# Kernel tuning notes

Measured on AMD Instinct MI355X. Metric: run time of the kernel, lower is better.

## Reference

```python
import jax, jax.numpy as jnp
import numpy as np
import math

NUM_HEADS = 16


def setup_inputs() -> dict:
    key = jax.random.key(0)
    ks = jax.random.split(key, 7)
    B, S, D = 2, 2048, 1024
    scale = 1.0 / math.sqrt(D)
    return {
        "query": jax.random.normal(ks[0], (B, S, D), jnp.float32),
        "key": jax.random.normal(ks[1], (B, S, D), jnp.float32),
        "value": jax.random.normal(ks[2], (B, S, D), jnp.float32),
        "Wq": jax.random.normal(ks[3], (D, D), jnp.float32) * scale,
        "Wk": jax.random.normal(ks[4], (D, D), jnp.float32) * scale,
        "Wv": jax.random.normal(ks[5], (D, D), jnp.float32) * scale,
        "Wo": jax.random.normal(ks[6], (D, D), jnp.float32) * scale,
    }


def reference(query, key, value, Wq, Wk, Wv, Wo):
    B, Sq, D = query.shape
    Sk = key.shape[1]
    H = NUM_HEADS
    dk = D // H
    # torch Linear (no bias): y = x @ W.T
    q = (query @ Wq.T).reshape(B, Sq, H, dk).transpose(0, 2, 1, 3)  # [B,H,Sq,dk]
    k = (key @ Wk.T).reshape(B, Sk, H, dk).transpose(0, 2, 1, 3)
    v = (value @ Wv.T).reshape(B, Sk, H, dk).transpose(0, 2, 1, 3)
    scores = jnp.einsum("bhqd,bhkd->bhqk", q, k) / jnp.sqrt(jnp.float32(dk))
    causal = jnp.tril(jnp.ones((Sq, Sk), dtype=bool))  # mask_future=True
    scores = jnp.where(causal[None, None], scores, jnp.float32(-1e9))
    p = jax.nn.softmax(scores, axis=-1)
    x = jnp.einsum("bhqk,bhkd->bhqd", p, v)  # [B,H,Sq,dk]
    x = x.transpose(0, 2, 1, 3).reshape(B, Sq, D)
    return x @ Wo.T
```

## Files before the change

kernel.cpp:

```cpp
#include <hip/hip_runtime.h>
#include <hip/hip_bf16.h>
#include <stdint.h>

#define D_MODEL 1024
#define NHEADS  16
#define DK      64
#define SEQ     2048
#define BATCH   2

typedef __bf16 bf16x8 __attribute__((ext_vector_type(8)));
typedef __bf16 bf16x4 __attribute__((ext_vector_type(4)));
typedef float  f32x4  __attribute__((ext_vector_type(4)));

__device__ __forceinline__ void async_copy16(const void* g, void* l) {
  __builtin_amdgcn_global_load_lds(
      (__attribute__((address_space(1))) void*)g,
      (__attribute__((address_space(3))) void*)l, 16, 0, 0);
}

__global__ void cast_all(const float* __restrict__ q, const float* __restrict__ k,
                         const float* __restrict__ v, const float* __restrict__ wq,
                         const float* __restrict__ wk, const float* __restrict__ wv,
                         const float* __restrict__ wo,
                         __bf16* __restrict__ oq, __bf16* __restrict__ ok,
                         __bf16* __restrict__ ov, __bf16* __restrict__ owq,
                         __bf16* __restrict__ owk, __bf16* __restrict__ owv,
                         __bf16* __restrict__ owo) {
  constexpr unsigned Q4 = (unsigned)(BATCH * SEQ * D_MODEL) / 4;
  constexpr unsigned W4 = (unsigned)(D_MODEL * D_MODEL) / 4;
  unsigned i = blockIdx.x * 256u + threadIdx.x;
  const float* in; __bf16* out; unsigned off;
  if (i < 3 * Q4) {
    unsigned z = i >> 20; off = i & (Q4 - 1);
    in  = z == 0 ? q : z == 1 ? k : v;
    out = z == 0 ? oq : z == 1 ? ok : ov;
  } else {
    unsigned j = i - 3 * Q4;
    unsigned z = j >> 18; off = j & (W4 - 1);
    in  = z == 0 ? wq : z == 1 ? wk : z == 2 ? wv : wo;
    out = z == 0 ? owq : z == 1 ? owk : z == 2 ? owv : owo;
  }
  float4 val = *(const float4*)(in + (size_t)off * 4);
  bf16x4 o;
  o.x = (__bf16)val.x; o.y = (__bf16)val.y; o.z = (__bf16)val.z; o.w = (__bf16)val.w;
  *(bf16x4*)(out + (size_t)off * 4) = o;
}

__global__ __launch_bounds__(256, 3)
void gemm_proj(const __bf16* __restrict__ A0, const __bf16* __restrict__ A1, const __bf16* __restrict__ A2,
               const __bf16* __restrict__ B0, const __bf16* __restrict__ B1, const __bf16* __restrict__ B2,
               __bf16* __restrict__ Qp, __bf16* __restrict__ Kp, __bf16* __restrict__ Vt) {
  constexpr int K = D_MODEL, N = D_MODEL;
  const int zi = blockIdx.z;
  const __bf16* A; const __bf16* Bm;
  if (zi == 0)      { A = A0; Bm = B0; }
  else if (zi == 1) { A = A1; Bm = B1; }
  else              { A = A2; Bm = B2; }

  __shared__ __align__(16) char smem[34816];
  __bf16* Ash = (__bf16*)smem;
  __bf16* Bsh = (__bf16*)(smem + 16384);
  __bf16* Tr  = (__bf16*)smem;

  const int tid  = threadIdx.x;
  const int lane = tid & 63;
  const int w    = tid >> 6;
  const int quad = lane >> 4;
  const int l16  = lane & 15;
  const int wr   = w >> 1, wc = w & 1;
  const size_t m0 = (size_t)blockIdx.x * 128;
  const size_t n0 = (size_t)blockIdx.y * 128;

  f32x4 acc[4][4] = {};

  for (int k0 = 0; k0 < K; k0 += 64) {
#pragma unroll
    for (int it = 0; it < 4; ++it) {
      int slot = tid + it * 256;
      int row = slot >> 3, ch = slot & 7;
      async_copy16(A + (m0 + row) * K + k0 + ((ch ^ (row & 7)) * 8), &Ash[slot * 8]);
    }
#pragma unroll
    for (int it = 0; it < 4; ++it) {
      int slot = tid + it * 256;
      int row = slot >> 3, ch = slot & 7;
      async_copy16(Bm + (n0 + row) * K + k0 + ((ch ^ (row & 7)) * 8), &Bsh[slot * 8]);
    }
    __syncthreads();
#pragma unroll
    for (int kk = 0; kk < 2; ++kk) {
      bf16x8 af[4], bfr[4];
#pragma unroll
      for (int i = 0; i < 4; ++i) {
        int row = wr * 64 + i * 16 + l16;
        af[i] = *(const bf16x8*)&Ash[row * 64 + (((kk * 4 + quad) ^ (row & 7)) * 8)];
      }
#pragma unroll
      for (int j = 0; j < 4; ++j) {
        int row = wc * 64 + j * 16 + l16;
        bfr[j] = *(const bf16x8*)&Bsh[row * 64 + (((kk * 4 + quad) ^ (row & 7)) * 8)];
      }
#pragma unroll
      for (int i = 0; i < 4; ++i)
#pragma unroll
        for (int j = 0; j < 4; ++j)
          acc[i][j] = __builtin_amdgcn_mfma_f32_16x16x32_bf16(af[i], bfr[j], acc[i][j], 0, 0, 0);
    }
    __syncthreads();
  }

  if (zi != 2) {
    __bf16* C = (zi == 0) ? Qp : Kp;
#pragma unroll
    for (int i = 0; i < 4; ++i)
#pragma unroll
      for (int j = 0; j < 4; ++j)
#pragma unroll
        for (int r = 0; r < 4; ++r) {
          size_t row = m0 + wr * 64 + i * 16 + quad * 4 + r;
          size_t col = n0 + wc * 64 + j * 16 + l16;
          C[row * N + col] = (__bf16)acc[i][j][r];
        }
  } else {
#pragma unroll
    for (int i = 0; i < 4; ++i)
#pragma unroll
      for (int j = 0; j < 4; ++j)
#pragma unroll
        for (int r = 0; r < 4; ++r)
          Tr[(wc * 64 + j * 16 + l16) * 136 + (wr * 64 + i * 16 + quad * 4 + r)] =
              (__bf16)acc[i][j][r];
    __syncthreads();
    const int b_  = (int)(m0 >> 11);
    const int sl0 = (int)(m0 & 2047);
#pragma unroll
    for (int it = 0; it < 8; ++it) {
      int slot = tid + it * 256;
      int d = slot >> 4, sc = slot & 15;
      *(int4*)&Vt[((size_t)(b_ * D_MODEL) + n0 + d) * SEQ + sl0 + sc * 8] =
          *(const int4*)&Tr[d * 136 + sc * 8];
    }
  }
}

__global__ __launch_bounds__(256, 2)
void gemm_out(const __bf16* __restrict__ A, const __bf16* __restrict__ Bm,
              float* __restrict__ C) {
  constexpr int BM = 64, BN = 128, K = D_MODEL, N = D_MODEL;
  __shared__ __bf16 Ash[BM * 64];
  __shared__ __bf16 Bsh[BN * 64];

  const int tid  = threadIdx.x;
  const int lane = tid & 63;
  const int w    = tid >> 6;
  const int quad = lane >> 4;
  const int l16  = lane & 15;
  const int wr   = w >> 1, wc = w & 1;
  const size_t m0 = (size_t)blockIdx.x * BM;
  const size_t n0 = (size_t)blockIdx.y * BN;

  f32x4 acc[2][4] = {};

  for (int k0 = 0; k0 < K; k0 += 64) {
#pragma unroll
    for (int it = 0; it < 2; ++it) {
      int slot = tid + it * 256;
      int row = slot >> 3, ch = slot & 7;
      async_copy16(A + (m0 + row) * K + k0 + ((ch ^ (row & 7)) * 8), &Ash[slot * 8]);
    }
#pragma unroll
    for (int it = 0; it < 4; ++it) {
      int slot = tid + it * 256;
      int row = slot >> 3, ch = slot & 7;
      async_copy16(Bm + (n0 + row) * K + k0 + ((ch ^ (row & 7)) * 8), &Bsh[slot * 8]);
    }
    __syncthreads();
#pragma unroll
    for (int kk = 0; kk < 2; ++kk) {
      bf16x8 af[2], bfr[4];
#pragma unroll
      for (int i = 0; i < 2; ++i) {
        int row = wr * 32 + i * 16 + l16;
        af[i] = *(const bf16x8*)&Ash[row * 64 + (((kk * 4 + quad) ^ (row & 7)) * 8)];
      }
#pragma unroll
      for (int j = 0; j < 4; ++j) {
        int row = wc * 64 + j * 16 + l16;
        bfr[j] = *(const bf16x8*)&Bsh[row * 64 + (((kk * 4 + quad) ^ (row & 7)) * 8)];
      }
#pragma unroll
      for (int i = 0; i < 2; ++i)
#pragma unroll
        for (int j = 0; j < 4; ++j)
          acc[i][j] = __builtin_amdgcn_mfma_f32_16x16x32_bf16(af[i], bfr[j], acc[i][j], 0, 0, 0);
    }
    __syncthreads();
  }

#pragma unroll
  for (int i = 0; i < 2; ++i)
#pragma unroll
    for (int j = 0; j < 4; ++j)
#pragma unroll
      for (int r = 0; r < 4; ++r) {
        size_t row = m0 + wr * 32 + i * 16 + quad * 4 + r;
        size_t col = n0 + wc * 64 + j * 16 + l16;
        C[row * N + col] = acc[i][j][r];
      }
}

__global__ __launch_bounds__(256, 4)
void attn_kernel(const __bf16* __restrict__ Qp, const __bf16* __restrict__ Kp,
                 const __bf16* __restrict__ Vt, __bf16* __restrict__ Xo) {
  __shared__ __align__(16) char smem[32768];
  __bf16* Kb = (__bf16*)smem;
  __bf16* Vb = (__bf16*)(smem + 16384);
  float*  Xch = (float*)smem;
  float*  Ls  = (float*)(smem + 8448);

  const int tid  = threadIdx.x;
  const int lane = tid & 63;
  const int w    = tid >> 6;
  const int qh   = w >> 1, kh = w & 1;
  const int quad = lane >> 4;
  const int l16  = lane & 15;
  const int bh   = blockIdx.x;
  const int qt   = 31 - blockIdx.y;
  const int b    = bh >> 4, h = bh & 15;
  const int q0   = qt * 64;
  const size_t baseRow = (size_t)b * SEQ;
  const int colBase = h * DK;

  const int srow = w * 16 + (lane >> 2);
  const int sk   = (lane & 3) * 8;
  const int skz  = (((lane & 3) ^ ((lane >> 3) & 3)) * 8);
  const int swz  = (l16 >> 1) & 3;

  const float c1 = 0.18033688011f;
  const float c2 = -23.083120654f;

  bf16x8 aq[2][2];
  {
    const __bf16* qrow = Qp + (baseRow + q0 + qh * 32 + l16) * D_MODEL + colBase;
#pragma unroll
    for (int mt = 0; mt < 2; ++mt)
#pragma unroll
      for (int kd = 0; kd < 2; ++kd)
        aq[mt][kd] = *(const bf16x8*)(qrow + (size_t)mt * 16 * D_MODEL + kd * 32 + quad * 8);
  }

  f32x4 oacc[2][4] = {};
  float plsum[2] = {};

  const int e1 = (((quad >> 1) ^ swz) * 8) + (quad & 1) * 4;
  const int e2 = ((((quad >> 1) + 2) ^ swz) * 8) + (quad & 1) * 4;

  {
    const __bf16* kbase = Kp + (baseRow + srow) * D_MODEL + colBase + skz;
    async_copy16(kbase,      &Kb[0 * 2048 + srow * 32 + sk]);
    async_copy16(kbase + 32, &Kb[1 * 2048 + srow * 32 + sk]);
    const __bf16* vbase = Vt + ((size_t)b * D_MODEL + colBase + srow) * SEQ + skz;
    async_copy16(vbase,      &Vb[0 * 2048 + srow * 32 + sk]);
    async_copy16(vbase + 32, &Vb[1 * 2048 + srow * 32 + sk]);
  }

  for (int j = 0; j <= qt; ++j) {
    const int bf = j & 1;
    __syncthreads();

    if (j < qt) {
      const int nb = bf ^ 1;
      const __bf16* kbase = Kp + (baseRow + (size_t)(j + 1) * 64 + srow) * D_MODEL + colBase + skz;
      async_copy16(kbase,      &Kb[(nb * 2 + 0) * 2048 + srow * 32 + sk]);
      async_copy16(kbase + 32, &Kb[(nb * 2 + 1) * 2048 + srow * 32 + sk]);
      const __bf16* vbase = Vt + ((size_t)b * D_MODEL + colBase + srow) * SEQ + (size_t)(j + 1) * 64 + skz;
      async_copy16(vbase,      &Vb[(nb * 2 + 0) * 2048 + srow * 32 + sk]);
      async_copy16(vbase + 32, &Vb[(nb * 2 + 1) * 2048 + srow * 32 + sk]);
    }

    f32x4 sacc[2][2] = {};
    __builtin_amdgcn_s_setprio(1);
#pragma unroll
    for (int kd = 0; kd < 2; ++kd) {
      bf16x8 bk0 = *(const bf16x8*)&Kb[(bf * 2 + kd) * 2048 + (kh * 32 + l16) * 32 + (quad ^ swz) * 8];
      bf16x8 bk1 = *(const bf16x8*)&Kb[(bf * 2 + kd) * 2048 + (kh * 32 + 16 + l16) * 32 + (quad ^ swz) * 8];
      sacc[0][0] = __builtin_amdgcn_mfma_f32_16x16x32_bf16(bk0, aq[0][kd], sacc[0][0], 0, 0, 0);
      sacc[0][1] = __builtin_amdgcn_mfma_f32_16x16x32_bf16(bk0, aq[1][kd], sacc[0][1], 0, 0, 0);
      sacc[1][0] = __builtin_amdgcn_mfma_f32_16x16x32_bf16(bk1, aq[0][kd], sacc[1][0], 0, 0, 0);
      sacc[1][1] = __builtin_amdgcn_mfma_f32_16x16x32_bf16(bk1, aq[1][kd], sacc[1][1], 0, 0, 0);
    }
    __builtin_amdgcn_s_setprio(0);

    const bool diag = (j == qt);
    bf16x8 pa[2];
#pragma unroll
    for (int mt = 0; mt < 2; ++mt)
#pragma unroll
      for (int st = 0; st < 2; ++st)
#pragma unroll
        for (int r = 0; r < 4; ++r) {
          float arg = fmaf(sacc[st][mt][r], c1, c2);
          if (diag) {
            int rowg = q0 + qh * 32 + mt * 16 + l16;
            int colg = j * 64 + kh * 32 + st * 16 + quad * 4 + r;
            if (colg > rowg) arg = -1e30f;
          }
          float p = __builtin_amdgcn_exp2f(arg);
          plsum[mt] += p;
          pa[mt][st * 4 + r] = (__bf16)p;
        }

    __builtin_amdgcn_s_setprio(1);
#pragma unroll
    for (int nt = 0; nt < 4; ++nt) {
      const int rowb = (bf * 2 + kh) * 2048 + (nt * 16 + l16) * 32;
      bf16x4 lo = *(const bf16x4*)&Vb[rowb + e1];
      bf16x4 hi = *(const bf16x4*)&Vb[rowb + e2];
      bf16x8 bv;
      bv[0] = lo[0]; bv[1] = lo[1]; bv[2] = lo[2]; bv[3] = lo[3];
      bv[4] = hi[0]; bv[5] = hi[1]; bv[6] = hi[2]; bv[7] = hi[3];
      oacc[0][nt] = __builtin_amdgcn_mfma_f32_16x16x32_bf16(pa[0], bv, oacc[0][nt], 0, 0, 0);
      oacc[1][nt] = __builtin_amdgcn_mfma_f32_16x16x32_bf16(pa[1], bv, oacc[1][nt], 0, 0, 0);
    }
    __builtin_amdgcn_s_setprio(0);
  }

  float lred[2];
#pragma unroll
  for (int mt = 0; mt < 2; ++mt) {
    float l = plsum[mt];
    l += __shfl_xor(l, 16, 64);
    l += __shfl_xor(l, 32, 64);
    lred[mt] = l;
  }

#pragma unroll
  for (int mt = 0; mt < 2; ++mt) {
    __syncthreads();
    if (kh == 1) {
#pragma unroll
      for (int nt = 0; nt < 4; ++nt)
#pragma unroll
        for (int r = 0; r < 4; ++r)
          Xch[(qh * 16 + quad * 4 + r) * 66 + nt * 16 + l16] = oacc[mt][nt][r];
    }
    if (quad == 0) Ls[kh * 32 + qh * 16 + l16] = lred[mt];
    __syncthreads();
    if (kh == 0) {
#pragma unroll
      for (int r = 0; r < 4; ++r) {
        float lt  = Ls[0 * 32 + qh * 16 + quad * 4 + r] + Ls[1 * 32 + qh * 16 + quad * 4 + r];
        float inv = 1.0f / lt;
        size_t row = baseRow + q0 + qh * 32 + mt * 16 + quad * 4 + r;
#pragma unroll
        for (int nt = 0; nt < 4; ++nt) {
          float o = oacc[mt][nt][r] + Xch[(qh * 16 + quad * 4 + r) * 66 + nt * 16 + l16];
          Xo[row * D_MODEL + colBase + nt * 16 + l16] = (__bf16)(o * inv);
        }
      }
    }
  }
}

extern "C" void kernel_launch(void* const* d_in, const int* in_sizes, int n_in,
                              void* d_out, int out_size, void* d_ws, size_t ws_size,
                              hipStream_t stream) {
  const float* q  = (const float*)d_in[0];
  const float* k  = (const float*)d_in[1];
  const float* v  = (const float*)d_in[2];
  const float* wq = (const float*)d_in[3];
  const float* wk = (const float*)d_in[4];
  const float* wv = (const float*)d_in[5];
  const float* wo = (const float*)d_in[6];
  float* out = (float*)d_out;

  const size_t MD = (size_t)BATCH * SEQ * D_MODEL;
  const size_t WD = (size_t)D_MODEL * D_MODEL;
  __bf16* ws  = (__bf16*)d_ws;
  __bf16* Qp  = ws;
  __bf16* Kp  = Qp + MD;
  __bf16* Vt  = Kp + MD;
  __bf16* Xa  = Vt + MD;
  __bf16* qbf = Xa + MD;
  __bf16* kbf = qbf + MD;
  __bf16* vbf = kbf + MD;
  __bf16* wqb = vbf + MD;
  __bf16* wkb = wqb + WD;
  __bf16* wvb = wkb + WD;
  __bf16* wob = wvb + WD;

  cast_all<<<16384, 256, 0, stream>>>(q, k, v, wq, wk, wv, wo,
                                      qbf, kbf, vbf, wqb, wkb, wvb, wob);

  gemm_proj<<<dim3(32, 8, 3), 256, 0, stream>>>(
      qbf, kbf, vbf, wqb, wkb, wvb, Qp, Kp, Vt);

  attn_kernel<<<dim3(BATCH * NHEADS, 32), 256, 0, stream>>>(Qp, Kp, Vt, Xa);

  gemm_out<<<dim3(64, 8), 256, 0, stream>>>(Xa, wob, out);
}
```

Baseline: 182.6 us.

## Fuse all four stages into one persistent cooperative kernel with grid syncs

Replaces the four separate launches (cast, QKV projection, attention, output projection) with one cooperative kernel of 768 blocks that runs each stage and separates them with grid.sync. Attention work is rebalanced: blocks 512 and up each take two causal tiles (one long, one short) to even out the triangular workload. The aim is to remove launch gaps and tail effects between kernels. In exchange it adds grid-wide barrier costs, limits occupancy to 3 blocks per CU, and leaves a quarter of the blocks idle during the output GEMM. A fallback to the old multi-kernel path is kept.

```diff
diff --git a/kernel.cpp b/kernel.cpp
--- a/kernel.cpp
+++ b/kernel.cpp
@@ -1,4 +1,5 @@
 #include <hip/hip_runtime.h>
+#include <hip/hip_cooperative_groups.h>
 #include <hip/hip_bf16.h>
 #include <stdint.h>
 
@@ -8,6 +9,8 @@
 #define SEQ     2048
 #define BATCH   2
 
+namespace cg = cooperative_groups;
+
 typedef __bf16 bf16x8 __attribute__((ext_vector_type(8)));
 typedef __bf16 bf16x4 __attribute__((ext_vector_type(4)));
 typedef float  f32x4  __attribute__((ext_vector_type(4)));
@@ -18,17 +21,17 @@
       (__attribute__((address_space(3))) void*)l, 16, 0, 0);
 }
 
-__global__ void cast_all(const float* __restrict__ q, const float* __restrict__ k,
-                         const float* __restrict__ v, const float* __restrict__ wq,
-                         const float* __restrict__ wk, const float* __restrict__ wv,
-                         const float* __restrict__ wo,
-                         __bf16* __restrict__ oq, __bf16* __restrict__ ok,
-                         __bf16* __restrict__ ov, __bf16* __restrict__ owq,
-                         __bf16* __restrict__ owk, __bf16* __restrict__ owv,
-                         __bf16* __restrict__ owo) {
+
+__device__ __forceinline__ void stage_cast(
+    unsigned i, const float* __restrict__ q, const float* __restrict__ k,
+    const float* __restrict__ v, const float* __restrict__ wq,
+    const float* __restrict__ wk, const float* __restrict__ wv,
+    const float* __restrict__ wo,
+    __bf16* __restrict__ oq, __bf16* __restrict__ ok, __bf16* __restrict__ ov,
+    __bf16* __restrict__ owq, __bf16* __restrict__ owk, __bf16* __restrict__ owv,
+    __bf16* __restrict__ owo) {
   constexpr unsigned Q4 = (unsigned)(BATCH * SEQ * D_MODEL) / 4;
   constexpr unsigned W4 = (unsigned)(D_MODEL * D_MODEL) / 4;
-  unsigned i = blockIdx.x * 256u + threadIdx.x;
   const float* in; __bf16* out; unsigned off;
   if (i < 3 * Q4) {
     unsigned z = i >> 20; off = i & (Q4 - 1);
@@ -46,18 +49,11 @@
   *(bf16x4*)(out + (size_t)off * 4) = o;
 }
 
-__global__ __launch_bounds__(256, 3)
-void gemm_proj(const __bf16* __restrict__ A0, const __bf16* __restrict__ A1, const __bf16* __restrict__ A2,
-               const __bf16* __restrict__ B0, const __bf16* __restrict__ B1, const __bf16* __restrict__ B2,
-               __bf16* __restrict__ Qp, __bf16* __restrict__ Kp, __bf16* __restrict__ Vt) {
+__device__ __forceinline__ void stage_proj(
+    char* smem, int zi, size_t m0, size_t n0,
+    const __bf16* __restrict__ A, const __bf16* __restrict__ Bm,
+    __bf16* __restrict__ Qp, __bf16* __restrict__ Kp, __bf16* __restrict__ Vt) {
   constexpr int K = D_MODEL, N = D_MODEL;
-  const int zi = blockIdx.z;
-  const __bf16* A; const __bf16* Bm;
-  if (zi == 0)      { A = A0; Bm = B0; }
-  else if (zi == 1) { A = A1; Bm = B1; }
-  else              { A = A2; Bm = B2; }
-
-  __shared__ __align__(16) char smem[34816];
   __bf16* Ash = (__bf16*)smem;
   __bf16* Bsh = (__bf16*)(smem + 16384);
   __bf16* Tr  = (__bf16*)smem;
@@ -68,8 +64,6 @@
   const int quad = lane >> 4;
   const int l16  = lane & 15;
   const int wr   = w >> 1, wc = w & 1;
-  const size_t m0 = (size_t)blockIdx.x * 128;
-  const size_t n0 = (size_t)blockIdx.y * 128;
 
   f32x4 acc[4][4] = {};
 
@@ -143,80 +137,16 @@
   }
 }
 
-__global__ __launch_bounds__(256, 2)
-void gemm_out(const __bf16* __restrict__ A, const __bf16* __restrict__ Bm,
-              float* __restrict__ C) {
-  constexpr int BM = 64, BN = 128, K = D_MODEL, N = D_MODEL;
-  __shared__ __bf16 Ash[BM * 64];
-  __shared__ __bf16 Bsh[BN * 64];
-
-  const int tid  = threadIdx.x;
-  const int lane = tid & 63;
-  const int w    = tid >> 6;
-  const int quad = lane >> 4;
-  const int l16  = lane & 15;
-  const int wr   = w >> 1, wc = w & 1;
-  const size_t m0 = (size_t)blockIdx.x * BM;
-  const size_t n0 = (size_t)blockIdx.y * BN;
-
-  f32x4 acc[2][4] = {};
-
-  for (int k0 = 0; k0 < K; k0 += 64) {
-#pragma unroll
-    for (int it = 0; it < 2; ++it) {
-      int slot = tid + it * 256;
-      int row = slot >> 3, ch = slot & 7;
-      async_copy16(A + (m0 + row) * K + k0 + ((ch ^ (row & 7)) * 8), &Ash[slot * 8]);
-    }
-#pragma unroll
-    for (int it = 0; it < 4; ++it) {
-      int slot = tid + it * 256;
-      int row = slot >> 3, ch = slot & 7;
-      async_copy16(Bm + (n0 + row) * K + k0 + ((ch ^ (row & 7)) * 8), &Bsh[slot * 8]);
-    }
-    __syncthreads();
-#pragma unroll
-    for (int kk = 0; kk < 2; ++kk) {
-      bf16x8 af[2], bfr[4];
-#pragma unroll
-      for (int i = 0; i < 2; ++i) {
-        int row = wr * 32 + i * 16 + l16;
-        af[i] = *(const bf16x8*)&Ash[row * 64 + (((kk * 4 + quad) ^ (row & 7)) * 8)];
-      }
-#pragma unroll
-      for (int j = 0; j < 4; ++j) {
-        int row = wc * 64 + j * 16 + l16;
-        bfr[j] = *(const bf16x8*)&Bsh[row * 64 + (((kk * 4 + quad) ^ (row & 7)) * 8)];
-      }
-#pragma unroll
-      for (int i = 0; i < 2; ++i)
-#pragma unroll
-        for (int j = 0; j < 4; ++j)
-          acc[i][j] = __builtin_amdgcn_mfma_f32_16x16x32_bf16(af[i], bfr[j], acc[i][j], 0, 0, 0);
-    }
-    __syncthreads();
-  }
-
-#pragma unroll
-  for (int i = 0; i < 2; ++i)
-#pragma unroll
-    for (int j = 0; j < 4; ++j)
-#pragma unroll
-      for (int r = 0; r < 4; ++r) {
-        size_t row = m0 + wr * 32 + i * 16 + quad * 4 + r;
-        size_t col = n0 + wc * 64 + j * 16 + l16;
-        C[row * N + col] = acc[i][j][r];
-      }
-}
-
-__global__ __launch_bounds__(256, 4)
-void attn_kernel(const __bf16* __restrict__ Qp, const __bf16* __restrict__ Kp,
-                 const __bf16* __restrict__ Vt, __bf16* __restrict__ Xo) {
-  __shared__ __align__(16) char smem[32768];
+__device__ __forceinline__ void stage_attn(
+    char* smem, int bh, int qt,
+    const __bf16* __restrict__ Qp, const __bf16* __restrict__ Kp,
+    const __bf16* __restrict__ Vt, __bf16* __restrict__ Xo) {
   __bf16* Kb = (__bf16*)smem;
   __bf16* Vb = (__bf16*)(smem + 16384);
   float*  Xch = (float*)smem;
   float*  Ls  = (float*)(smem + 8448);
+
+  __syncthreads();
 
   const int tid  = threadIdx.x;
   const int lane = tid & 63;
@@ -224,8 +154,6 @@
   const int qh   = w >> 1, kh = w & 1;
   const int quad = lane >> 4;
   const int l16  = lane & 15;
-  const int bh   = blockIdx.x;
-  const int qt   = 31 - blockIdx.y;
   const int b    = bh >> 4, h = bh & 15;
   const int q0   = qt * 64;
   const size_t baseRow = (size_t)b * SEQ;
@@ -360,6 +288,156 @@
       }
     }
   }
+}
+
+__device__ __forceinline__ void stage_out(
+    char* smem, size_t m0, size_t n0,
+    const __bf16* __restrict__ A, const __bf16* __restrict__ Bm,
+    float* __restrict__ C) {
+  constexpr int K = D_MODEL, N = D_MODEL;
+  __bf16* Ash = (__bf16*)smem;
+  __bf16* Bsh = (__bf16*)(smem + 8192);
+
+  const int tid  = threadIdx.x;
+  const int lane = tid & 63;
+  const int w    = tid >> 6;
+  const int quad = lane >> 4;
+  const int l16  = lane & 15;
+  const int wr   = w >> 1, wc = w & 1;
+
+  f32x4 acc[2][4] = {};
+
+  for (int k0 = 0; k0 < K; k0 += 64) {
+#pragma unroll
+    for (int it = 0; it < 2; ++it) {
+      int slot = tid + it * 256;
+      int row = slot >> 3, ch = slot & 7;
+      async_copy16(A + (m0 + row) * K + k0 + ((ch ^ (row & 7)) * 8), &Ash[slot * 8]);
+    }
+#pragma unroll
+    for (int it = 0; it < 4; ++it) {
+      int slot = tid + it * 256;
+      int row = slot >> 3, ch = slot & 7;
+      async_copy16(Bm + (n0 + row) * K + k0 + ((ch ^ (row & 7)) * 8), &Bsh[slot * 8]);
+    }
+    __syncthreads();
+#pragma unroll
+    for (int kk = 0; kk < 2; ++kk) {
+      bf16x8 af[2], bfr[4];
+#pragma unroll
+      for (int i = 0; i < 2; ++i) {
+        int row = wr * 32 + i * 16 + l16;
+        af[i] = *(const bf16x8*)&Ash[row * 64 + (((kk * 4 + quad) ^ (row & 7)) * 8)];
+      }
+#pragma unroll
+      for (int j = 0; j < 4; ++j) {
+        int row = wc * 64 + j * 16 + l16;
+        bfr[j] = *(const bf16x8*)&Bsh[row * 64 + (((kk * 4 + quad) ^ (row & 7)) * 8)];
+      }
+#pragma unroll
+      for (int i = 0; i < 2; ++i)
+#pragma unroll
+        for (int j = 0; j < 4; ++j)
+          acc[i][j] = __builtin_amdgcn_mfma_f32_16x16x32_bf16(af[i], bfr[j], acc[i][j], 0, 0, 0);
+    }
+    __syncthreads();
+  }
+
+#pragma unroll
+  for (int i = 0; i < 2; ++i)
+#pragma unroll
+    for (int j = 0; j < 4; ++j)
+#pragma unroll
+      for (int r = 0; r < 4; ++r) {
+        size_t row = m0 + wr * 32 + i * 16 + quad * 4 + r;
+        size_t col = n0 + wc * 64 + j * 16 + l16;
+        C[row * N + col] = acc[i][j][r];
+      }
+}
+
+__global__ __launch_bounds__(256, 3)
+void fused_all(const float* __restrict__ q, const float* __restrict__ k,
+               const float* __restrict__ v, const float* __restrict__ wq,
+               const float* __restrict__ wk, const float* __restrict__ wv,
+               const float* __restrict__ wo,
+               __bf16* __restrict__ qbf, __bf16* __restrict__ kbf, __bf16* __restrict__ vbf,
+               __bf16* __restrict__ wqb, __bf16* __restrict__ wkb, __bf16* __restrict__ wvb,
+               __bf16* __restrict__ wob,
+               __bf16* __restrict__ Qp, __bf16* __restrict__ Kp, __bf16* __restrict__ Vt,
+               __bf16* __restrict__ Xa, float* __restrict__ out) {
+  __shared__ __align__(16) char smem[34816];
+  cg::grid_group grid = cg::this_grid();
+  const unsigned bid = blockIdx.x;
+
+  {
+    constexpr unsigned total = 4u << 20;
+    for (unsigned i = bid * 256u + threadIdx.x; i < total; i += 768u * 256u)
+      stage_cast(i, q, k, v, wq, wk, wv, wo, qbf, kbf, vbf, wqb, wkb, wvb, wob);
+  }
+  grid.sync();
+
+  {
+    const int zi = bid >> 8;
+    const int rem = bid & 255;
+    const __bf16* A  = zi == 0 ? qbf : zi == 1 ? kbf : vbf;
+    const __bf16* Bm = zi == 0 ? wqb : zi == 1 ? wkb : wvb;
+    stage_proj(smem, zi, (size_t)(rem & 31) * 128, (size_t)(rem >> 5) * 128,
+               A, Bm, Qp, Kp, Vt);
+  }
+  grid.sync();
+
+  {
+    if (bid < 512) {
+      stage_attn(smem, (int)(bid & 31), 31 - (int)(bid >> 5), Qp, Kp, Vt, Xa);
+    } else {
+      const int p = (int)bid - 512;
+      const int bh = p & 31, jj = p >> 5;
+      stage_attn(smem, bh, 15 - jj, Qp, Kp, Vt, Xa);
+      stage_attn(smem, bh, jj,      Qp, Kp, Vt, Xa);
+    }
+  }
+  grid.sync();
+
+  if (bid < 512)
+    stage_out(smem, (size_t)(bid & 63) * 64, (size_t)(bid >> 6) * 128, Xa, wob, out);
+}
+
+
+__global__ void cast_all(const float* __restrict__ q, const float* __restrict__ k,
+                         const float* __restrict__ v, const float* __restrict__ wq,
+                         const float* __restrict__ wk, const float* __restrict__ wv,
+                         const float* __restrict__ wo,
+                         __bf16* __restrict__ oq, __bf16* __restrict__ ok,
+                         __bf16* __restrict__ ov, __bf16* __restrict__ owq,
+                         __bf16* __restrict__ owk, __bf16* __restrict__ owv,
+                         __bf16* __restrict__ owo) {
+  unsigned i = blockIdx.x * 256u + threadIdx.x;
+  stage_cast(i, q, k, v, wq, wk, wv, wo, oq, ok, ov, owq, owk, owv, owo);
+}
+
+__global__ __launch_bounds__(256, 3)
+void gemm_proj(const __bf16* __restrict__ A0, const __bf16* __restrict__ A1, const __bf16* __restrict__ A2,
+               const __bf16* __restrict__ B0, const __bf16* __restrict__ B1, const __bf16* __restrict__ B2,
+               __bf16* __restrict__ Qp, __bf16* __restrict__ Kp, __bf16* __restrict__ Vt) {
+  __shared__ __align__(16) char smem[34816];
+  const int zi = blockIdx.z;
+  const __bf16* A  = zi == 0 ? A0 : zi == 1 ? A1 : A2;
+  const __bf16* Bm = zi == 0 ? B0 : zi == 1 ? B1 : B2;
+  stage_proj(smem, zi, (size_t)blockIdx.x * 128, (size_t)blockIdx.y * 128, A, Bm, Qp, Kp, Vt);
+}
+
+__global__ __launch_bounds__(256, 4)
+void attn_kernel(const __bf16* __restrict__ Qp, const __bf16* __restrict__ Kp,
+                 const __bf16* __restrict__ Vt, __bf16* __restrict__ Xo) {
+  __shared__ __align__(16) char smem[32768];
+  stage_attn(smem, (int)blockIdx.x, 31 - (int)blockIdx.y, Qp, Kp, Vt, Xo);
+}
+
+__global__ __launch_bounds__(256, 2)
+void gemm_out(const __bf16* __restrict__ A, const __bf16* __restrict__ Bm,
+              float* __restrict__ C) {
+  __shared__ __align__(16) char smem[24576];
+  stage_out(smem, (size_t)blockIdx.x * 64, (size_t)blockIdx.y * 128, A, Bm, C);
 }
 
 extern "C" void kernel_launch(void* const* d_in, const int* in_sizes, int n_in,
@@ -389,13 +467,30 @@
   __bf16* wvb = wkb + WD;
   __bf16* wob = wvb + WD;
 
-  cast_all<<<16384, 256, 0, stream>>>(q, k, v, wq, wk, wv, wo,
-                                      qbf, kbf, vbf, wqb, wkb, wvb, wob);
-
-  gemm_proj<<<dim3(32, 8, 3), 256, 0, stream>>>(
-      qbf, kbf, vbf, wqb, wkb, wvb, Qp, Kp, Vt);
-
-  attn_kernel<<<dim3(BATCH * NHEADS, 32), 256, 0, stream>>>(Qp, Kp, Vt, Xa);
-
-  gemm_out<<<dim3(64, 8), 256, 0, stream>>>(Xa, wob, out);
-}
+  static int coop_state = -1;
+  if (coop_state < 0) {
+    int nb = 0;
+    hipError_t e = hipOccupancyMaxActiveBlocksPerMultiprocessor(&nb, fused_all, 256, 0);
+    coop_state = (e == hipSuccess && nb >= 3) ? 1 : 0;
+  }
+
+  bool done = false;
+  if (coop_state == 1) {
+    void* args[] = {
+      (void*)&q, (void*)&k, (void*)&v, (void*)&wq, (void*)&wk, (void*)&wv, (void*)&wo,
+      (void*)&qbf, (void*)&kbf, (void*)&vbf, (void*)&wqb, (void*)&wkb, (void*)&wvb, (void*)&wob,
+      (void*)&Qp, (void*)&Kp, (void*)&Vt, (void*)&Xa, (void*)&out
+    };
+    hipError_t e = hipLaunchCooperativeKernel(fused_all, dim3(768), dim3(256), args, 0, stream);
+    if (e == hipSuccess) done = true; else coop_state = 0;
+  }
+
+  if (!done) {
+    cast_all<<<16384, 256, 0, stream>>>(q, k, v, wq, wk, wv, wo,
+                                        qbf, kbf, vbf, wqb, wkb, wvb, wob);
+    gemm_proj<<<dim3(32, 8, 3), 256, 0, stream>>>(
+        qbf, kbf, vbf, wqb, wkb, wvb, Qp, Kp, Vt);
+    attn_kernel<<<dim3(BATCH * NHEADS, 32), 256, 0, stream>>>(Qp, Kp, Vt, Xa);
+    gemm_out<<<dim3(64, 8), 256, 0, stream>>>(Xa, wob, out);
+  }
+}
```

Result: no change. 183.1 us (+0.3%).

## Process two 64-key tiles per barrier step in attention kernel

Applied to the files above, without the earlier changes.

The attention loop now loads 128 keys of K and V per pipeline stage into a doubled 64KB shared buffer and processes them as two 64-key sub-tiles. This halves the number of __syncthreads and prefetch rounds per query tile and issues larger batches of async loads. In exchange, LDS use doubles and launch bounds drop from 4 to 2 blocks per CU, which lowers occupancy. The last stage may over-fetch a tile beyond the causal limit, and that tile is skipped at compute time.

```diff
diff --git a/kernel.cpp b/kernel.cpp
--- a/kernel.cpp
+++ b/kernel.cpp
@@ -209,12 +209,12 @@
       }
 }
 
-__global__ __launch_bounds__(256, 4)
+__global__ __launch_bounds__(256, 2)
 void attn_kernel(const __bf16* __restrict__ Qp, const __bf16* __restrict__ Kp,
                  const __bf16* __restrict__ Vt, __bf16* __restrict__ Xo) {
-  __shared__ __align__(16) char smem[32768];
+  __shared__ __align__(16) char smem[65536];
   __bf16* Kb = (__bf16*)smem;
-  __bf16* Vb = (__bf16*)(smem + 16384);
+  __bf16* Vb = (__bf16*)(smem + 32768);
   float*  Xch = (float*)smem;
   float*  Ls  = (float*)(smem + 8448);
 
@@ -255,74 +255,90 @@
   const int e1 = (((quad >> 1) ^ swz) * 8) + (quad & 1) * 4;
   const int e2 = ((((quad >> 1) + 2) ^ swz) * 8) + (quad & 1) * 4;
 
+  const int nsteps = (qt + 2) >> 1;
+
   {
-    const __bf16* kbase = Kp + (baseRow + srow) * D_MODEL + colBase + skz;
-    async_copy16(kbase,      &Kb[0 * 2048 + srow * 32 + sk]);
-    async_copy16(kbase + 32, &Kb[1 * 2048 + srow * 32 + sk]);
-    const __bf16* vbase = Vt + ((size_t)b * D_MODEL + colBase + srow) * SEQ + skz;
-    async_copy16(vbase,      &Vb[0 * 2048 + srow * 32 + sk]);
-    async_copy16(vbase + 32, &Vb[1 * 2048 + srow * 32 + sk]);
-  }
-
-  for (int j = 0; j <= qt; ++j) {
+    const __bf16* kb0 = Kp + (baseRow + srow) * D_MODEL + colBase + skz;
+    async_copy16(kb0,                    &Kb[0 * 2048 + srow * 32 + sk]);
+    async_copy16(kb0 + 32,               &Kb[1 * 2048 + srow * 32 + sk]);
+    async_copy16(kb0 + 64 * D_MODEL,     &Kb[2 * 2048 + srow * 32 + sk]);
+    async_copy16(kb0 + 64 * D_MODEL + 32,&Kb[3 * 2048 + srow * 32 + sk]);
+    const __bf16* vb0 = Vt + ((size_t)b * D_MODEL + colBase + srow) * SEQ + skz;
+    async_copy16(vb0,      &Vb[0 * 2048 + srow * 32 + sk]);
+    async_copy16(vb0 + 32, &Vb[1 * 2048 + srow * 32 + sk]);
+    async_copy16(vb0 + 64, &Vb[2 * 2048 + srow * 32 + sk]);
+    async_copy16(vb0 + 96, &Vb[3 * 2048 + srow * 32 + sk]);
+  }
+
+  for (int j = 0; j < nsteps; ++j) {
     const int bf = j & 1;
     __syncthreads();
 
-    if (j < qt) {
+    if (j + 1 < nsteps) {
       const int nb = bf ^ 1;
-      const __bf16* kbase = Kp + (baseRow + (size_t)(j + 1) * 64 + srow) * D_MODEL + colBase + skz;
-      async_copy16(kbase,      &Kb[(nb * 2 + 0) * 2048 + srow * 32 + sk]);
-      async_copy16(kbase + 32, &Kb[(nb * 2 + 1) * 2048 + srow * 32 + sk]);
-      const __bf16* vbase = Vt + ((size_t)b * D_MODEL + colBase + srow) * SEQ + (size_t)(j + 1) * 64 + skz;
-      async_copy16(vbase,      &Vb[(nb * 2 + 0) * 2048 + srow * 32 + sk]);
-      async_copy16(vbase + 32, &Vb[(nb * 2 + 1) * 2048 + srow * 32 + sk]);
-    }
-
-    f32x4 sacc[2][2] = {};
-    __builtin_amdgcn_s_setprio(1);
-#pragma unroll
-    for (int kd = 0; kd < 2; ++kd) {
-      bf16x8 bk0 = *(const bf16x8*)&Kb[(bf * 2 + kd) * 2048 + (kh * 32 + l16) * 32 + (quad ^ swz) * 8];
-      bf16x8 bk1 = *(const bf16x8*)&Kb[(bf * 2 + kd) * 2048 + (kh * 32 + 16 + l16) * 32 + (quad ^ swz) * 8];
-      sacc[0][0] = __builtin_amdgcn_mfma_f32_16x16x32_bf16(bk0, aq[0][kd], sacc[0][0], 0, 0, 0);
-      sacc[0][1] = __builtin_amdgcn_mfma_f32_16x16x32_bf16(bk0, aq[1][kd], sacc[0][1], 0, 0, 0);
-      sacc[1][0] = __builtin_amdgcn_mfma_f32_16x16x32_bf16(bk1, aq[0][kd], sacc[1][0], 0, 0, 0);
-      sacc[1][1] = __builtin_amdgcn_mfma_f32_16x16x32_bf16(bk1, aq[1][kd], sacc[1][1], 0, 0, 0);
-    }
-    __builtin_amdgcn_s_setprio(0);
-
-    const bool diag = (j == qt);
-    bf16x8 pa[2];
-#pragma unroll
-    for (int mt = 0; mt < 2; ++mt)
-#pragma unroll
-      for (int st = 0; st < 2; ++st)
-#pragma unroll
-        for (int r = 0; r < 4; ++r) {
-          float arg = fmaf(sacc[st][mt][r], c1, c2);
-          if (diag) {
-            int rowg = q0 + qh * 32 + mt * 16 + l16;
-            int colg = j * 64 + kh * 32 + st * 16 + quad * 4 + r;
-            if (colg > rowg) arg = -1e30f;
-          }
-          float p = __builtin_amdgcn_exp2f(arg);
-          plsum[mt] += p;
-          pa[mt][st * 4 + r] = (__bf16)p;
+      const __bf16* kb0 = Kp + (baseRow + (size_t)(j + 1) * 128 + srow) * D_MODEL + colBase + skz;
+      async_copy16(kb0,                    &Kb[(nb * 4 + 0) * 2048 + srow * 32 + sk]);
+      async_copy16(kb0 + 32,               &Kb[(nb * 4 + 1) * 2048 + srow * 32 + sk]);
+      async_copy16(kb0 + 64 * D_MODEL,     &Kb[(nb * 4 + 2) * 2048 + srow * 32 + sk]);
+      async_copy16(kb0 + 64 * D_MODEL + 32,&Kb[(nb * 4 + 3) * 2048 + srow * 32 + sk]);
+      const __bf16* vb0 = Vt + ((size_t)b * D_MODEL + colBase + srow) * SEQ + (size_t)(j + 1) * 128 + skz;
+      async_copy16(vb0,      &Vb[(nb * 4 + 0) * 2048 + srow * 32 + sk]);
+      async_copy16(vb0 + 32, &Vb[(nb * 4 + 1) * 2048 + srow * 32 + sk]);
+      async_copy16(vb0 + 64, &Vb[(nb * 4 + 2) * 2048 + srow * 32 + sk]);
+      async_copy16(vb0 + 96, &Vb[(nb * 4 + 3) * 2048 + srow * 32 + sk]);
+    }
+
+#pragma unroll
+    for (int sub = 0; sub < 2; ++sub) {
+      const int scb = j * 128 + sub * 64;
+      if (scb <= q0) {
+        f32x4 sacc[2][2] = {};
+        __builtin_amdgcn_s_setprio(1);
+#pragma unroll
+        for (int kd = 0; kd < 2; ++kd) {
+          bf16x8 bk0 = *(const bf16x8*)&Kb[(bf * 4 + sub * 2 + kd) * 2048 + (kh * 32 + l16) * 32 + (quad ^ swz) * 8];
+          bf16x8 bk1 = *(const bf16x8*)&Kb[(bf * 4 + sub * 2 + kd) * 2048 + (kh * 32 + 16 + l16) * 32 + (quad ^ swz) * 8];
+          sacc[0][0] = __builtin_amdgcn_mfma_f32_16x16x32_bf16(bk0, aq[0][kd], sacc[0][0], 0, 0, 0);
+          sacc[0][1] = __builtin_amdgcn_mfma_f32_16x16x32_bf16(bk0, aq[1][kd], sacc[0][1], 0, 0, 0);
+          sacc[1][0] = __builtin_amdgcn_mfma_f32_16x16x32_bf16(bk1, aq[0][kd], sacc[1][0], 0, 0, 0);
+          sacc[1][1] = __builtin_amdgcn_mfma_f32_16x16x32_bf16(bk1, aq[1][kd], sacc[1][1], 0, 0, 0);
         }
-
-    __builtin_amdgcn_s_setprio(1);
-#pragma unroll
-    for (int nt = 0; nt < 4; ++nt) {
-      const int rowb = (bf * 2 + kh) * 2048 + (nt * 16 + l16) * 32;
-      bf16x4 lo = *(const bf16x4*)&Vb[rowb + e1];
-      bf16x4 hi = *(const bf16x4*)&Vb[rowb + e2];
-      bf16x8 bv;
-      bv[0] = lo[0]; bv[1] = lo[1]; bv[2] = lo[2]; bv[3] = lo[3];
-      bv[4] = hi[0]; bv[5] = hi[1]; bv[6] = hi[2]; bv[7] = hi[3];
-      oacc[0][nt] = __builtin_amdgcn_mfma_f32_16x16x32_bf16(pa[0], bv, oacc[0][nt], 0, 0, 0);
-      oacc[1][nt] = __builtin_amdgcn_mfma_f32_16x16x32_bf16(pa[1], bv, oacc[1][nt], 0, 0, 0);
-    }
-    __builtin_amdgcn_s_setprio(0);
+        __builtin_amdgcn_s_setprio(0);
+
+        const bool diag = (scb == q0);
+        bf16x8 pa[2];
+#pragma unroll
+        for (int mt = 0; mt < 2; ++mt)
+#pragma unroll
+          for (int st = 0; st < 2; ++st)
+#pragma unroll
+            for (int r = 0; r < 4; ++r) {
+              float arg = fmaf(sacc[st][mt][r], c1, c2);
+              if (diag) {
+                int rowg = q0 + qh * 32 + mt * 16 + l16;
+                int colg = scb + kh * 32 + st * 16 + quad * 4 + r;
+                if (colg > rowg) arg = -1e30f;
+              }
+              float p = __builtin_amdgcn_exp2f(arg);
+              plsum[mt] += p;
+              pa[mt][st * 4 + r] = (__bf16)p;
+            }
+
+        __builtin_amdgcn_s_setprio(1);
+#pragma unroll
+        for (int nt = 0; nt < 4; ++nt) {
+          const int rowb = (bf * 4 + sub * 2 + kh) * 2048 + (nt * 16 + l16) * 32;
+          bf16x4 lo = *(const bf16x4*)&Vb[rowb + e1];
+          bf16x4 hi = *(const bf16x4*)&Vb[rowb + e2];
+          bf16x8 bv;
+          bv[0] = lo[0]; bv[1] = lo[1]; bv[2] = lo[2]; bv[3] = lo[3];
+          bv[4] = hi[0]; bv[5] = hi[1]; bv[6] = hi[2]; bv[7] = hi[3];
+          oacc[0][nt] = __builtin_amdgcn_mfma_f32_16x16x32_bf16(pa[0], bv, oacc[0][nt], 0, 0, 0);
+          oacc[1][nt] = __builtin_amdgcn_mfma_f32_16x16x32_bf16(pa[1], bv, oacc[1][nt], 0, 0, 0);
+        }
+        __builtin_amdgcn_s_setprio(0);
+      }
+    }
   }
 
   float lred[2];
```

Result: slower. 186.8 us (+2.3%).
